# Performance work log

Hardware: AMD Instinct MI355X
Metric: run time of the kernel (lower is better)

Reference implementation:

```python
import jax, jax.numpy as jnp
import numpy as np

N = 200000
E = 500000
F_IN = 165
HID = 256
N_CLASSES = 2


def setup_inputs() -> dict:
    key = jax.random.key(0)
    ks = jax.random.split(key, 8)
    x = jax.random.normal(ks[0], (N, F_IN), dtype=jnp.float32)
    edge_index = jax.random.randint(ks[1], (2, E), 0, N, dtype=jnp.int64)
    # PyG SAGEConv params: lin_l applied to mean-aggregated neighbors (with bias),
    # lin_r applied to root features (no bias). Glorot-ish init scale.
    def lin(k, fin, fout):
        return jax.random.normal(k, (fin, fout), dtype=jnp.float32) / np.sqrt(fin)
    return {
        "x": x,
        "edge_index": edge_index,
        "w1_l": lin(ks[2], F_IN, HID),
        "w1_r": lin(ks[3], F_IN, HID),
        "b1": jnp.zeros((HID,), dtype=jnp.float32),
        "w2_l": lin(ks[4], HID, N_CLASSES),
        "w2_r": lin(ks[5], HID, N_CLASSES),
        "b2": jnp.zeros((N_CLASSES,), dtype=jnp.float32),
    }


def _sage_conv(x, edge_index, w_l, w_r, b):
    # PyG SAGEConv with default mean aggregation:
    #   out = lin_l(mean_{j in N(i)} x_j) + lin_r(x_i) + b
    src, dst = edge_index[0], edge_index[1]
    n = x.shape[0]
    deg = jax.ops.segment_sum(jnp.ones((src.shape[0],), x.dtype), dst, num_segments=n)
    agg = jax.ops.segment_sum(x[src], dst, num_segments=n)  # [N, F]
    agg = agg / jnp.maximum(deg, 1.0)[:, None]
    return agg @ w_l + x @ w_r + b


def reference(x, edge_index, w1_l, w1_r, b1, w2_l, w2_r, b2):
    h = jax.nn.relu(_sage_conv(x, edge_index, w1_l, w1_r, b1))
    # F.dropout(training=self.training) is identity in eval mode.
    logits = _sage_conv(h, edge_index, w2_l, w2_r, b2)
    return (logits, edge_index)
```

## Files before the change

### kernel.cpp

```cpp
#include <hip/hip_runtime.h>
#include <hip/hip_bf16.h>
#include <hip/hip_fp16.h>

#define N_NODES 200000
#define N_EDGES 500000
#define F_IN    165
#define HID     256
#define SX      192
#define NB      782

typedef float    floatx4 __attribute__((ext_vector_type(4)));
typedef float    floatx4a __attribute__((ext_vector_type(4), aligned(16)));
typedef _Float16 half8   __attribute__((ext_vector_type(8)));

__global__ void cast_x_kernel(const float* __restrict__ x, __half2* __restrict__ xh) {
    int idx = blockIdx.x * blockDim.x + threadIdx.x;
    int row = idx / 96;
    int p = idx - row * 96;
    int f0 = 2 * p;
    float v0 = (f0 < F_IN) ? x[(long)row * F_IN + f0] : 0.0f;
    float v1 = (f0 + 1 < F_IN) ? x[(long)row * F_IN + f0 + 1] : 0.0f;
    xh[idx] = __floats2half2_rn(v0, v1);
}

__global__ void hist_kernel(const int* __restrict__ ei, int* __restrict__ degi) {
    int e = blockIdx.x * blockDim.x + threadIdx.x;
    if (e < N_EDGES) atomicAdd(&degi[ei[N_EDGES + e]], 1);
}

__global__ __launch_bounds__(256) void block_sum_kernel(const int* __restrict__ degi,
                                                        int* __restrict__ bsum) {
    __shared__ int sh[256];
    int t = threadIdx.x, i = blockIdx.x * 256 + t;
    sh[t] = (i < N_NODES) ? degi[i] : 0;
    __syncthreads();
#pragma unroll
    for (int off = 128; off > 0; off >>= 1) {
        if (t < off) sh[t] += sh[t + off];
        __syncthreads();
    }
    if (t == 0) bsum[blockIdx.x] = sh[0];
}

__global__ __launch_bounds__(1024) void scan_bsum_kernel(const int* __restrict__ bsum,
                                                         int* __restrict__ boff,
                                                         int* __restrict__ row_start) {
    __shared__ int sh[1024];
    int t = threadIdx.x;
    int v = (t < NB) ? bsum[t] : 0;
    sh[t] = v;
    __syncthreads();
    for (int off = 1; off < 1024; off <<= 1) {
        int u = (t >= off) ? sh[t - off] : 0;
        __syncthreads();
        sh[t] += u;
        __syncthreads();
    }
    if (t < NB) boff[t] = sh[t] - v;
    if (t == 1023) row_start[N_NODES] = sh[1023];
}

__global__ __launch_bounds__(256) void scan_emit_kernel(const int* __restrict__ degi,
                                                        const int* __restrict__ boff,
                                                        int* __restrict__ row_start,
                                                        int* __restrict__ cursor,
                                                        float* __restrict__ invdeg) {
    __shared__ int sh[256];
    int t = threadIdx.x, i = blockIdx.x * 256 + t;
    int d = (i < N_NODES) ? degi[i] : 0;
    sh[t] = d;
    __syncthreads();
#pragma unroll
    for (int off = 1; off < 256; off <<= 1) {
        int u = (t >= off) ? sh[t - off] : 0;
        __syncthreads();
        sh[t] += u;
        __syncthreads();
    }
    if (i < N_NODES) {
        int row = boff[blockIdx.x] + sh[t] - d;
        row_start[i] = row;
        cursor[i] = row;
        invdeg[i] = 1.0f / fmaxf((float)d, 1.0f);
    }
}

__global__ void scatter_edges_kernel(const int* __restrict__ ei,
                                     int* __restrict__ cursor,
                                     int* __restrict__ csr) {
    int e = blockIdx.x * blockDim.x + threadIdx.x;
    if (e >= N_EDGES) return;
    int s = ei[e];
    int d = ei[N_EDGES + e];
    int pos = atomicAdd(&cursor[d], 1);
    csr[pos] = s;
}

__global__ void gather_agg_kernel(const __half2* __restrict__ xh,
                                  const int* __restrict__ row_start,
                                  const int* __restrict__ csr,
                                  __half2* __restrict__ aggh) {
    int idx = blockIdx.x * blockDim.x + threadIdx.x;
    int n = idx / 96;
    int p = idx - n * 96;
    int e0 = row_start[n], e1 = row_start[n + 1];
    float sx = 0.f, sy = 0.f;
    for (int e = e0; e < e1; ++e) {
        int s = csr[e];
        float2 f = __half22float2(xh[(long)s * 96 + p]);
        sx += f.x; sy += f.y;
    }
    aggh[idx] = __floats2half2_rn(sx, sy);
}

__global__ void prep_bfrag_kernel(const float* __restrict__ w1l,
                                  const float* __restrict__ w1r,
                                  _Float16* __restrict__ bfrag) {
    int gid = blockIdx.x * blockDim.x + threadIdx.x;
    if (gid >= 12 * 16 * 64) return;
    int lane = gid & 63;
    int j = (gid >> 6) & 15;
    int c = gid >> 10;
    int quad = lane >> 4, n = lane & 15;
    const float* w = (c < 6) ? w1l : w1r;
    int kb = (c < 6 ? c : c - 6) * 32;
    int col = j * 16 + n;
    half8 r;
#pragma unroll
    for (int q = 0; q < 8; ++q) {
        int k = kb + quad * 8 + q;
        r[q] = (_Float16)((k < F_IN) ? w[k * HID + col] : 0.0f);
    }
    *(half8*)(bfrag + gid * 8) = r;
}

__global__ __launch_bounds__(512, 2) void gemm_fused_kernel(
        const _Float16* __restrict__ xh, const _Float16* __restrict__ aggh,
        const float* __restrict__ invdeg, const _Float16* __restrict__ bfrag,
        const float* __restrict__ b1,
        const float* __restrict__ w2l, const float* __restrict__ w2r,
        float* __restrict__ tl, float* __restrict__ tr) {
    __shared__ float tlr[128][4];
    const int tid = threadIdx.x;
    const int w = tid >> 6, lane = tid & 63;
    const int quad = lane >> 4, l15 = lane & 15;
    const int mrow0 = blockIdx.x * 128 + (w & 1) * 64;
    const int jbase = (w >> 1) * 4;

    ((float*)tlr)[tid < 512 ? tid : 0] = 0.0f;
    __syncthreads();

    int  rows[4];
    bool rv[4];
#pragma unroll
    for (int i = 0; i < 4; ++i) {
        rows[i] = mrow0 + i * 16 + l15;
        rv[i] = rows[i] < N_NODES;
    }

    floatx4 acc[4][4];
#pragma unroll
    for (int i = 0; i < 4; ++i)
#pragma unroll
        for (int jj = 0; jj < 4; ++jj)
            acc[i][jj] = (floatx4){0.f, 0.f, 0.f, 0.f};

    const half8 zero8 = {0, 0, 0, 0, 0, 0, 0, 0};

#pragma unroll 2
    for (int c = 0; c < 12; ++c) {
        const _Float16* __restrict__ src = (c < 6) ? aggh : xh;
        const int kb = (c < 6 ? c : c - 6) * 32;
        half8 a[4], b[4];
#pragma unroll
        for (int i = 0; i < 4; ++i)
            a[i] = rv[i] ? *(const half8*)(src + (long)rows[i] * SX + kb + quad * 8)
                         : zero8;
#pragma unroll
        for (int jj = 0; jj < 4; ++jj)
            b[jj] = *(const half8*)(bfrag + (((c * 16) + jbase + jj) * 64 + lane) * 8);
#pragma unroll
        for (int i = 0; i < 4; ++i)
#pragma unroll
            for (int jj = 0; jj < 4; ++jj)
                acc[i][jj] = __builtin_amdgcn_mfma_f32_16x16x32_f16(a[i], b[jj], acc[i][jj], 0, 0, 0);

        if (c == 5) {
#pragma unroll
            for (int i = 0; i < 4; ++i) {
                int rb = mrow0 + i * 16 + quad * 4;
                floatx4 iv;
                if (rb + 3 < N_NODES) {
                    iv = *(const floatx4a*)(invdeg + rb);
                } else {
#pragma unroll
                    for (int t = 0; t < 4; ++t)
                        iv[t] = (rb + t < N_NODES) ? invdeg[rb + t] : 0.0f;
                }
#pragma unroll
                for (int jj = 0; jj < 4; ++jj)
                    acc[i][jj] *= iv;
            }
        }
    }

    float bb[4], wl0[4], wl1[4], wr0[4], wr1[4];
#pragma unroll
    for (int jj = 0; jj < 4; ++jj) {
        int col = (w >> 1) * 64 + jj * 16 + l15;
        bb[jj]  = b1[col];
        wl0[jj] = w2l[col * 2];  wl1[jj] = w2l[col * 2 + 1];
        wr0[jj] = w2r[col * 2];  wr1[jj] = w2r[col * 2 + 1];
    }
#pragma unroll
    for (int i = 0; i < 4; ++i) {
#pragma unroll
        for (int t = 0; t < 4; ++t) {
            float s0 = 0.f, s1 = 0.f, s2 = 0.f, s3 = 0.f;
#pragma unroll
            for (int jj = 0; jj < 4; ++jj) {
                float v = fmaxf(acc[i][jj][t] + bb[jj], 0.0f);
                s0 += v * wl0[jj]; s1 += v * wl1[jj];
                s2 += v * wr0[jj]; s3 += v * wr1[jj];
            }
#pragma unroll
            for (int m = 1; m < 16; m <<= 1) {
                s0 += __shfl_xor(s0, m, 64);
                s1 += __shfl_xor(s1, m, 64);
                s2 += __shfl_xor(s2, m, 64);
                s3 += __shfl_xor(s3, m, 64);
            }
            if (l15 == 0) {
                int rl = (w & 1) * 64 + i * 16 + quad * 4 + t;
                atomicAdd(&tlr[rl][0], s0);
                atomicAdd(&tlr[rl][1], s1);
                atomicAdd(&tlr[rl][2], s2);
                atomicAdd(&tlr[rl][3], s3);
            }
        }
    }
    __syncthreads();
    if (tid < 128) {
        int row = blockIdx.x * 128 + tid;
        if (row < N_NODES) {
            tl[row * 2 + 0] = tlr[tid][0];
            tl[row * 2 + 1] = tlr[tid][1];
            tr[row * 2 + 0] = tlr[tid][2];
            tr[row * 2 + 1] = tlr[tid][3];
        }
    }
}

__global__ void gather_out_kernel(const int* __restrict__ row_start,
                                  const int* __restrict__ csr,
                                  const float* __restrict__ tl,
                                  const float* __restrict__ tr,
                                  const float* __restrict__ invdeg,
                                  const float* __restrict__ b2,
                                  float* __restrict__ out) {
    int i = blockIdx.x * blockDim.x + threadIdx.x;
    if (i >= N_NODES) return;
    int e0 = row_start[i], e1 = row_start[i + 1];
    float a0 = 0.f, a1 = 0.f;
    for (int e = e0; e < e1; ++e) {
        int s = csr[e];
        a0 += tl[s * 2 + 0];
        a1 += tl[s * 2 + 1];
    }
    float inv = invdeg[i];
    out[i * 2 + 0] = a0 * inv + tr[i * 2 + 0] + b2[0];
    out[i * 2 + 1] = a1 * inv + tr[i * 2 + 1] + b2[1];
}

__global__ void cast_edges_kernel(const int* __restrict__ ei,
                                  float* __restrict__ out) {
    int i = blockIdx.x * blockDim.x + threadIdx.x;
    if (i < 2 * N_EDGES) out[i] = (float)ei[i];
}

extern "C" void kernel_launch(void* const* d_in, const int* in_sizes, int n_in,
                              void* d_out, int out_size, void* d_ws, size_t ws_size,
                              hipStream_t stream) {
    const float* x    = (const float*)d_in[0];
    const int*   ei   = (const int*)d_in[1];
    const float* w1_l = (const float*)d_in[2];
    const float* w1_r = (const float*)d_in[3];
    const float* b1   = (const float*)d_in[4];
    const float* w2_l = (const float*)d_in[5];
    const float* w2_r = (const float*)d_in[6];
    const float* b2   = (const float*)d_in[7];

    char* ws = (char*)d_ws;
    int*   degi      = (int*)(ws);
    int*   row_start = (int*)(ws + 800000);
    int*   cursor    = (int*)(ws + 1600032);
    float* invdeg    = (float*)(ws + 2400032);
    int*   csr       = (int*)(ws + 3200032);
    float* tl        = (float*)(ws + 5200032);
    float* tr        = (float*)(ws + 6800032);
    int*   bsum      = (int*)(ws + 8400032);
    int*   boff      = (int*)(ws + 8403232);
    _Float16* bfrag  = (_Float16*)(ws + 8406432);
    _Float16* aggh   = (_Float16*)(ws + 8610000);
    _Float16* xh     = (_Float16*)(ws + 85410000);

    float* out = (float*)d_out;

    (void)hipMemsetAsync(degi, 0, 800000, stream);

    cast_x_kernel<<<75000, 256, 0, stream>>>(x, (__half2*)xh);
    prep_bfrag_kernel<<<48, 256, 0, stream>>>(w1_l, w1_r, bfrag);

    hist_kernel<<<(N_EDGES + 255) / 256, 256, 0, stream>>>(ei, degi);
    block_sum_kernel<<<NB, 256, 0, stream>>>(degi, bsum);
    scan_bsum_kernel<<<1, 1024, 0, stream>>>(bsum, boff, row_start);
    scan_emit_kernel<<<NB, 256, 0, stream>>>(degi, boff, row_start, cursor, invdeg);
    scatter_edges_kernel<<<(N_EDGES + 255) / 256, 256, 0, stream>>>(ei, cursor, csr);

    gather_agg_kernel<<<75000, 256, 0, stream>>>((const __half2*)xh, row_start, csr,
                                                 (__half2*)aggh);

    gemm_fused_kernel<<<(N_NODES + 127) / 128, 512, 0, stream>>>(
        xh, aggh, invdeg, bfrag, b1, w2_l, w2_r, tl, tr);

    gather_out_kernel<<<NB, 256, 0, stream>>>(row_start, csr, tl, tr, invdeg, b2, out);
    cast_edges_kernel<<<(2 * N_EDGES + 255) / 256, 256, 0, stream>>>(ei, out + 2 * N_NODES);
}
```

Baseline: 505.9 us.

## Stage A tiles in LDS via global_load_lds with swizzled layout

```diff
diff --git a/kernel.cpp b/kernel.cpp
--- a/kernel.cpp
+++ b/kernel.cpp
@@ -140,23 +140,23 @@
         const float* __restrict__ b1,
         const float* __restrict__ w2l, const float* __restrict__ w2r,
         float* __restrict__ tl, float* __restrict__ tr) {
+    __shared__ __attribute__((aligned(16))) _Float16 As[2][128 * 32];
     __shared__ float tlr[128][4];
     const int tid = threadIdx.x;
     const int w = tid >> 6, lane = tid & 63;
     const int quad = lane >> 4, l15 = lane & 15;
-    const int mrow0 = blockIdx.x * 128 + (w & 1) * 64;
+    const int rowbase = blockIdx.x * 128;
+    const int mrow0 = rowbase + (w & 1) * 64;
+    const int rhalf = (w & 1) * 64;
     const int jbase = (w >> 1) * 4;
 
     ((float*)tlr)[tid < 512 ? tid : 0] = 0.0f;
-    __syncthreads();
-
-    int  rows[4];
-    bool rv[4];
-#pragma unroll
-    for (int i = 0; i < 4; ++i) {
-        rows[i] = mrow0 + i * 16 + l15;
-        rv[i] = rows[i] < N_NODES;
-    }
+
+    const int srow_l = tid >> 2;
+    const int sseg = (tid & 3) ^ ((srow_l >> 1) & 3);
+    int srow = rowbase + srow_l;
+    if (srow >= N_NODES) srow = N_NODES - 1;
+    const long sgoff = (long)srow * SX + sseg * 8;
 
     floatx4 acc[4][4];
 #pragma unroll
@@ -165,43 +165,61 @@
         for (int jj = 0; jj < 4; ++jj)
             acc[i][jj] = (floatx4){0.f, 0.f, 0.f, 0.f};
 
-    const half8 zero8 = {0, 0, 0, 0, 0, 0, 0, 0};
-
-#pragma unroll 2
-    for (int c = 0; c < 12; ++c) {
-        const _Float16* __restrict__ src = (c < 6) ? aggh : xh;
-        const int kb = (c < 6 ? c : c - 6) * 32;
-        half8 a[4], b[4];
-#pragma unroll
-        for (int i = 0; i < 4; ++i)
-            a[i] = rv[i] ? *(const half8*)(src + (long)rows[i] * SX + kb + quad * 8)
-                         : zero8;
-#pragma unroll
-        for (int jj = 0; jj < 4; ++jj)
-            b[jj] = *(const half8*)(bfrag + (((c * 16) + jbase + jj) * 64 + lane) * 8);
-#pragma unroll
-        for (int i = 0; i < 4; ++i)
+    __syncthreads();
+
+#pragma unroll 1
+    for (int it = 0; it < 6; ++it) {
+#pragma unroll
+        for (int u = 0; u < 2; ++u) {
+            const int cc = it * 2 + u;
+            const _Float16* __restrict__ src = (cc < 6) ? aggh : xh;
+            const int kb = (cc < 6 ? cc : cc - 6) * 32;
+            const _Float16* gp = src + sgoff + kb;
+            char* dst = (char*)(&As[u][0]) + (tid & ~63) * 16;
+            __builtin_amdgcn_global_load_lds(
+                (const __attribute__((address_space(1))) void*)gp,
+                (__attribute__((address_space(3))) void*)dst, 16, 0, 0);
+        }
+        __syncthreads();
+
+#pragma unroll
+        for (int u = 0; u < 2; ++u) {
+            const int cc = it * 2 + u;
+            half8 a[4], b[4];
+#pragma unroll
+            for (int i = 0; i < 4; ++i) {
+                int r = rhalf + i * 16 + l15;
+                int slot = r * 4 + (quad ^ ((r >> 1) & 3));
+                a[i] = *(const half8*)(&As[u][slot * 8]);
+            }
 #pragma unroll
             for (int jj = 0; jj < 4; ++jj)
-                acc[i][jj] = __builtin_amdgcn_mfma_f32_16x16x32_f16(a[i], b[jj], acc[i][jj], 0, 0, 0);
-
-        if (c == 5) {
-#pragma unroll
-            for (int i = 0; i < 4; ++i) {
-                int rb = mrow0 + i * 16 + quad * 4;
-                floatx4 iv;
-                if (rb + 3 < N_NODES) {
-                    iv = *(const floatx4a*)(invdeg + rb);
-                } else {
-#pragma unroll
-                    for (int t = 0; t < 4; ++t)
-                        iv[t] = (rb + t < N_NODES) ? invdeg[rb + t] : 0.0f;
+                b[jj] = *(const half8*)(bfrag + (((cc * 16) + jbase + jj) * 64 + lane) * 8);
+#pragma unroll
+            for (int i = 0; i < 4; ++i)
+#pragma unroll
+                for (int jj = 0; jj < 4; ++jj)
+                    acc[i][jj] = __builtin_amdgcn_mfma_f32_16x16x32_f16(a[i], b[jj], acc[i][jj], 0, 0, 0);
+
+            if (cc == 5) {
+#pragma unroll
+                for (int i = 0; i < 4; ++i) {
+                    int rb = mrow0 + i * 16 + quad * 4;
+                    floatx4 iv;
+                    if (rb + 3 < N_NODES) {
+                        iv = *(const floatx4a*)(invdeg + rb);
+                    } else {
+#pragma unroll
+                        for (int t = 0; t < 4; ++t)
+                            iv[t] = (rb + t < N_NODES) ? invdeg[rb + t] : 0.0f;
+                    }
+#pragma unroll
+                    for (int jj = 0; jj < 4; ++jj)
+                        acc[i][jj] *= iv;
                 }
-#pragma unroll
-                for (int jj = 0; jj < 4; ++jj)
-                    acc[i][jj] *= iv;
             }
         }
+        __syncthreads();
     }
 
     float bb[4], wl0[4], wl1[4], wr0[4], wr1[4];
@@ -241,7 +259,7 @@
     }
     __syncthreads();
     if (tid < 128) {
-        int row = blockIdx.x * 128 + tid;
+        int row = rowbase + tid;
         if (row < N_NODES) {
             tl[row * 2 + 0] = tlr[tid][0];
             tl[row * 2 + 1] = tlr[tid][1];
```

Result: faster. 483.7 us (-4.4%).
